# Performance work log

Measured on AMD Instinct MI355X. Metric: run time of the kernel, lower is better.

## Reference

```python
import jax, jax.numpy as jnp
import numpy as np

IMG = 224; PATCH = 16; IN_CH = 3; EMBED = 768
ANCHORS = [(1, 1), (2, 2), (3, 3)]; A = len(ANCHORS)
STRIDE_TOTAL = 16; P = PATCH // STRIDE_TOTAL            # p = 1
PN = IMG // PATCH                                       # 14 patches per side
FH = IMG // STRIDE_TOTAL                                # 14x14 embedding map
G = max(max(a) for a in ANCHORS) * P                    # max roi sampling grid = 3
N = A * PN * PN                                         # 588 anchor scores
J = int((1 - 1 / A) * N)                                # 392 zeroed, matches torch int()
K = N - J                                               # 196 kept boxes
B = 16


def _roi_boxes():
    boxes = []
    for (ah, aw) in ANCHORS:
        h = ah * P; w = aw * P
        for i in range(PN):
            for j in range(PN):
                cy = (P - 1) / 2 + i * P
                cx = (P - 1) / 2 + j * P
                boxes.append([cy - h / 2, cx - w / 2, cy + h / 2, cx + w / 2])
    return np.asarray(boxes, np.float32)

ROI_BOXES = jnp.asarray(_roi_boxes())  # [N, 4], torchvision order (x1,y1,x2,y2)


def conv(x, w, b, s, p):
    y = jax.lax.conv_general_dilated(x, w, (s, s), [(p, p), (p, p)],
                                     dimension_numbers=('NCHW', 'OIHW', 'NCHW'))
    return y + b[None, :, None, None]


def bn(x, g, b, eps=1e-5):
    # training-mode batch norm (biased variance), as in the torch forward
    m = x.mean((0, 2, 3), keepdims=True)
    v = ((x - m) ** 2).mean((0, 2, 3), keepdims=True)
    return g[None, :, None, None] * (x - m) * jax.lax.rsqrt(v + eps) + b[None, :, None, None]


def roi_align_1x1(feat, boxes):
    # torchvision.ops.roi_align, output_size=(1,1), spatial_scale=1, sampling_ratio=-1, aligned=False
    # feat: [B, C, H, W], boxes: [B, K, 4] in (x1, y1, x2, y2)
    Bb, C, H, W = feat.shape
    bx1, by1, bx2, by2 = (boxes[..., i] for i in range(4))
    rw = jnp.maximum(bx2 - bx1, 1.0)
    rh = jnp.maximum(by2 - by1, 1.0)
    gh = jnp.ceil(rh).astype(jnp.int32)                 # adaptive sampling grid
    gw = jnp.ceil(rw).astype(jnp.int32)
    cnt = (gh * gw).astype(feat.dtype)                  # [B, K]
    ii = jnp.arange(G, dtype=feat.dtype)
    ys = by1[..., None] + (ii + 0.5) * rh[..., None] / gh[..., None].astype(feat.dtype)  # [B,K,G]
    xs = bx1[..., None] + (ii + 0.5) * rw[..., None] / gw[..., None].astype(feat.dtype)
    y = jnp.broadcast_to(ys[..., :, None], ys.shape[:-1] + (G, G))  # [B,K,G,G]
    x = jnp.broadcast_to(xs[..., None, :], xs.shape[:-1] + (G, G))
    gmask = (jnp.arange(G)[:, None] < gh[..., None, None]) & (jnp.arange(G)[None, :] < gw[..., None, None])
    valid = (y >= -1.0) & (y <= H) & (x >= -1.0) & (x <= W)
    yc = jnp.maximum(y, 0.0); xc = jnp.maximum(x, 0.0)
    yf = jnp.floor(yc).astype(jnp.int32); xf = jnp.floor(xc).astype(jnp.int32)
    ycap = yf >= H - 1; xcap = xf >= W - 1
    y_lo = jnp.where(ycap, H - 1, yf); y_hi = jnp.where(ycap, H - 1, yf + 1)
    x_lo = jnp.where(xcap, W - 1, xf); x_hi = jnp.where(xcap, W - 1, xf + 1)
    ly = jnp.where(ycap, 0.0, yc - yf.astype(feat.dtype))
    lx = jnp.where(xcap, 0.0, xc - xf.astype(feat.dtype))
    w11 = (1 - ly) * (1 - lx); w12 = (1 - ly) * lx
    w21 = ly * (1 - lx);       w22 = ly * lx
    ff = feat.reshape(Bb, C, H * W)
    gat = jax.vmap(lambda f, i: jnp.take(f, i, axis=-1))  # [C,HW],[K,G,G] -> [C,K,G,G]
    def g(yy, xx):
        return gat(ff, yy * W + xx)
    val = (w11[:, None] * g(y_lo, x_lo) + w12[:, None] * g(y_lo, x_hi)
           + w21[:, None] * g(y_hi, x_lo) + w22[:, None] * g(y_hi, x_hi))
    val = val * (valid & gmask)[:, None].astype(feat.dtype)   # [B,C,K,G,G]
    out = val.sum((-1, -2)) / cnt[:, None, :]                 # [B,C,K]
    return out.transpose(0, 2, 1)                             # [B,K,C]


def _forward(x, pw1, pb1, pw2, pb2, pw3, pb3,
             rw1, rb1, g1, b1, rw2, rb2, g2, b2, rw3, rb3, g3, b3, rw4, rb4):
    Bb = x.shape[0]
    # patch-embed conv stack (no activations, matches nn.Sequential of convs)
    e = conv(x, pw1, pb1, 4, 0)
    e = conv(e, pw2, pb2, 2, 0)
    e = conv(e, pw3, pb3, 2, 0)                    # [B, 768, 14, 14]
    # RPN scoring
    r = jax.nn.relu(bn(conv(x, rw1, rb1, 2, 1), g1, b1))
    r = jax.nn.relu(bn(conv(r, rw2, rb2, 2, 1), g2, b2))
    r = jax.nn.relu(bn(conv(r, rw3, rb3, 2, 1), g3, b3))
    score = conv(r, rw4, rb4, 2, 1)                # [B, A, 14, 14]
    s = score.reshape(Bb, -1)                      # [B, N]
    idx = jnp.argsort(s, axis=-1)                  # ascending, like torch.sort
    onehot = jnp.zeros_like(s).at[jnp.arange(Bb)[:, None], idx].set(
        jnp.broadcast_to((jnp.arange(N) >= J).astype(s.dtype), (Bb, N)))
    sm = jax.nn.softmax(s, axis=1)
    ste = jax.lax.stop_gradient(onehot - sm) + sm  # straight-through estimator
    sel = idx[:, J:]                               # [B, K] kept box ids
    boxes = ROI_BOXES[sel]                         # [B, K, 4]
    emb = roi_align_1x1(e, boxes)                  # [B, K, 768]
    gate = jnp.take_along_axis(ste, sel, axis=1)   # [B, K]
    return emb * gate[..., None]


def setup_inputs():
    key = jax.random.key(0)
    ks = jax.random.split(key, 16)
    def rn(i, shape, s=0.05):
        return jax.random.normal(ks[i], shape, jnp.float32) * s
    return {
        'x': jax.random.normal(ks[0], (B, IN_CH, IMG, IMG), jnp.float32),
        'pw1': rn(1, (64, 3, 4, 4)), 'pb1': rn(2, (64,)),
        'pw2': rn(3, (128, 64, 2, 2)), 'pb2': rn(4, (128,)),
        'pw3': rn(5, (EMBED, 128, 2, 2)), 'pb3': rn(6, (EMBED,)),
        'rw1': rn(7, (64, 3, 3, 3)), 'rb1': rn(8, (64,)),
        'g1': jnp.ones((64,), jnp.float32), 'b1': jnp.zeros((64,), jnp.float32),
        'rw2': rn(9, (128, 64, 3, 3)), 'rb2': rn(10, (128,)),
        'g2': jnp.ones((128,), jnp.float32), 'b2': jnp.zeros((128,), jnp.float32),
        'rw3': rn(11, (256, 128, 3, 3)), 'rb3': rn(12, (256,)),
        'g3': jnp.ones((256,), jnp.float32), 'b3': jnp.zeros((256,), jnp.float32),
        'rw4': rn(13, (A, 256, 3, 3)), 'rb4': rn(14, (A,)),
    }


def reference(x, pw1, pb1, pw2, pb2, pw3, pb3,
              rw1, rb1, g1, b1, rw2, rb2, g2, b2, rw3, rb3, g3, b3, rw4, rb4):
    return _forward(x, pw1, pb1, pw2, pb2, pw3, pb3,
                    rw1, rb1, g1, b1, rw2, rb2, g2, b2, rw3, rb3, g3, b3, rw4, rb4)
```

## Files before the change

kernel.cpp:

```cpp
#include <hip/hip_runtime.h>
#include <math.h>

#define BB 16
#define NBOX 588
#define TOPJ 392
#define TOPK 196
#define EMBED 768
#define NBLK 256

typedef unsigned short u16;
typedef unsigned int   u32;
using short8 = __attribute__((ext_vector_type(8))) short;
using f32x4  = __attribute__((ext_vector_type(4))) float;

__device__ inline u16 rnebf(float x) {
    u32 u = __builtin_bit_cast(u32, x);
    u32 r = u + 0x7fff + ((u >> 16) & 1);
    return (u16)(r >> 16);
}
__device__ inline float bfval(u16 h) {
    u32 u = ((u32)h) << 16;
    return __builtin_bit_cast(float, u);
}
__device__ inline u32 hi2(u32 w0, u32 w1) { return (w0 >> 16) | (w1 & 0xffff0000u); }
__device__ inline u32 lo2(u32 w0, u32 w1) { return (w0 & 0xffffu) | (w1 << 16); }

__global__ void w_split_all(
    const float* __restrict__ rw1, const float* __restrict__ rw2,
    const float* __restrict__ rw3, const float* __restrict__ rw4,
    const float* __restrict__ pw1, const float* __restrict__ pw2,
    const float* __restrict__ pw3,
    float* t1, float* t4, float* q1,
    u16* w2h, u16* w2m, u16* w2l,
    u16* w3h, u16* w3m, u16* w3l,
    u16* p2h, u16* p2l, u16* p3h, u16* p3l)
{
    int i = blockIdx.x * 256 + threadIdx.x;
    if (i < 1728) {
        int oc = i % 64; int k = i / 64; int tap = k % 9; int ic = k / 9;
        t1[i] = rw1[(oc * 3 + ic) * 9 + tap];
        return;
    }
    i -= 1728;
    if (i < 73728) {
        int oc = i / 576; int rem = i - oc * 576; int tap = rem >> 6; int ic = rem & 63;
        float v = rw2[(oc * 64 + ic) * 9 + tap];
        u16 h = rnebf(v); float r = v - bfval(h);
        u16 m = rnebf(r); float r2 = r - bfval(m);
        w2h[i] = h; w2m[i] = m; w2l[i] = rnebf(r2);
        return;
    }
    i -= 73728;
    if (i < 294912) {
        int oc = i / 1152; int rem = i - oc * 1152; int tap = rem >> 7; int ic = rem & 127;
        float v = rw3[(oc * 128 + ic) * 9 + tap];
        u16 h = rnebf(v); float r = v - bfval(h);
        u16 m = rnebf(r); float r2 = r - bfval(m);
        w3h[i] = h; w3m[i] = m; w3l[i] = rnebf(r2);
        return;
    }
    i -= 294912;
    if (i < 6912) {
        int ic = i % 256; int t = i / 256; int tap = t % 9; int oc = t / 9;
        t4[i] = rw4[(oc * 256 + ic) * 9 + tap];
        return;
    }
    i -= 6912;
    if (i < 3072) {
        int oc = i % 64; int k = i / 64; int tap = k % 16; int ic = k / 16;
        q1[i] = pw1[(oc * 3 + ic) * 16 + tap];
        return;
    }
    i -= 3072;
    if (i < 32768) {
        int oc = i >> 8; int rem = i & 255; int tap = rem >> 6; int ic = rem & 63;
        float v = pw2[(oc * 64 + ic) * 4 + tap];
        u16 h = rnebf(v);
        p2h[i] = h; p2l[i] = rnebf(v - bfval(h));
        return;
    }
    i -= 32768;
    if (i < 393216) {
        int oc = i >> 9; int rem = i & 511; int tap = rem >> 7; int ic = rem & 127;
        float v = pw3[(oc * 128 + ic) * 4 + tap];
        u16 h = rnebf(v);
        p3h[i] = h; p3l[i] = rnebf(v - bfval(h));
        return;
    }
}

__global__ void split3_bn(float* __restrict__ x, u16* __restrict__ lp,
                          const float* __restrict__ coef, int Cmask, long n4) {
    long i = (long)blockIdx.x * 256 + threadIdx.x;
    if (i >= n4) return;
    float4 v = *reinterpret_cast<const float4*>(x + i * 4);
    int c0 = (int)((i * 4) & Cmask);
    float4 sc = *reinterpret_cast<const float4*>(coef + c0);
    float4 sh = *reinterpret_cast<const float4*>(coef + (Cmask + 1) + c0);
    float y[4] = {fmaxf(fmaf(v.x, sc.x, sh.x), 0.f), fmaxf(fmaf(v.y, sc.y, sh.y), 0.f),
                  fmaxf(fmaf(v.z, sc.z, sh.z), 0.f), fmaxf(fmaf(v.w, sc.w, sh.w), 0.f)};
    u32 w[4]; u16 l[4];
#pragma unroll
    for (int j = 0; j < 4; ++j) {
        u16 h = rnebf(y[j]); float r = y[j] - bfval(h);
        u16 m = rnebf(r);    float r2 = r - bfval(m);
        l[j] = rnebf(r2);
        w[j] = ((u32)h << 16) | (u32)m;
    }
    uint4 wv; wv.x = w[0]; wv.y = w[1]; wv.z = w[2]; wv.w = w[3];
    *reinterpret_cast<uint4*>(x + i * 4) = wv;
    uint2 lv; lv.x = (u32)l[0] | ((u32)l[1] << 16); lv.y = (u32)l[2] | ((u32)l[3] << 16);
    *reinterpret_cast<uint2*>(lp + i * 4) = lv;
}

__global__ void split2_plain(float* __restrict__ x, long n4) {
    long i = (long)blockIdx.x * 256 + threadIdx.x;
    if (i >= n4) return;
    float4 v = *reinterpret_cast<const float4*>(x + i * 4);
    float y[4] = {v.x, v.y, v.z, v.w};
    u32 w[4];
#pragma unroll
    for (int j = 0; j < 4; ++j) {
        u16 h = rnebf(y[j]);
        u16 l = rnebf(y[j] - bfval(h));
        w[j] = ((u32)h << 16) | (u32)l;
    }
    uint4 wv; wv.x = w[0]; wv.y = w[1]; wv.z = w[2]; wv.w = w[3];
    *reinterpret_cast<uint4*>(x + i * 4) = wv;
}

template<int KH, int KW, int S, int P, int OCT>
__global__ __launch_bounds__(256) void conv_direct_nhwc(
    const float* __restrict__ in, const float* __restrict__ wT,
    const float* __restrict__ bias, float* __restrict__ out,
    int Cin, int Hin, int Win, int Cout, int Hout, int Wout)
{
    const int hw = Hout * Wout;
    const long total = (long)BB * hw;
    long sp = (long)blockIdx.x * 256 + threadIdx.x;
    if (sp >= total) return;
    int b  = (int)(sp / hw);
    int r  = (int)(sp - (long)b * hw);
    int oy = r / Wout;
    int ox = r - oy * Wout;
    int oc0 = blockIdx.y * OCT;

    float acc[OCT];
#pragma unroll
    for (int i = 0; i < OCT; ++i) acc[i] = bias[oc0 + i];

    int  ixc[KW]; long yoff[KH]; float xm[KW], ym[KH];
#pragma unroll
    for (int kx = 0; kx < KW; ++kx) {
        int ix = ox * S - P + kx;
        xm[kx] = (ix >= 0 && ix < Win) ? 1.f : 0.f;
        ixc[kx] = min(max(ix, 0), Win - 1);
    }
#pragma unroll
    for (int ky = 0; ky < KH; ++ky) {
        int iy = oy * S - P + ky;
        ym[ky] = (iy >= 0 && iy < Hin) ? 1.f : 0.f;
        yoff[ky] = (long)min(max(iy, 0), Hin - 1) * Win;
    }

    const float* ib = in + (long)b * Cin * Hin * Win;
    for (int ic = 0; ic < Cin; ++ic) {
        const float* ip = ib + (long)ic * Hin * Win;
#pragma unroll
        for (int ky = 0; ky < KH; ++ky) {
            const float* row = ip + yoff[ky];
#pragma unroll
            for (int kx = 0; kx < KW; ++kx) {
                float v = row[ixc[kx]];
                if (P > 0) v *= ym[ky] * xm[kx];
                const float* wr = wT + ((long)((ic * KH + ky) * KW + kx)) * Cout + oc0;
#pragma unroll
                for (int i = 0; i < OCT; ++i) acc[i] = fmaf(v, wr[i], acc[i]);
            }
        }
    }
    float* op = out + sp * Cout + oc0;
#pragma unroll
    for (int i = 0; i < OCT; i += 4) {
        float4 v = {acc[i], acc[i+1], acc[i+2], acc[i+3]};
        *reinterpret_cast<float4*>(op + i) = v;
    }
}

#define MBM 64
#define MBN 64
template<int KH, int KW, int S, int P, int CLOG, int NS, bool STATS>
__global__ __launch_bounds__(256, 6) void mfma_conv7(
    const u32* __restrict__ hm, const u16* __restrict__ lp,
    const u16* __restrict__ w0, const u16* __restrict__ w1, const u16* __restrict__ w2,
    const float* __restrict__ bias, float* __restrict__ out,
    float* __restrict__ psum, float* __restrict__ psq, int NT,
    int Hin, int Win, int Cout, int Hout, int Wout)
{
    const int Cin = 1 << CLOG;
    const int KK = KH * KW;
    const int Ktot = Cin * KK;
    const int hw = Hout * Wout;
    const long Mtot = (long)BB * hw;

    const int nwg = gridDim.x;
    const int orig = blockIdx.x;
    const int xcd = orig & 7, pos = orig >> 3;
    const int qc = nwg >> 3, rc = nwg & 7;
    const int logical = (xcd < rc ? xcd * (qc + 1) : rc * (qc + 1) + (xcd - rc) * qc) + pos;
    const int MT = nwg / NT;
    const int mt = logical / NT;
    const int nt = logical - mt * NT;
    const int n0 = nt * MBN;
    const long m0 = (long)mt * MBM;

    __shared__ u16 Asm[NS][MBM * 32];
    __shared__ u16 Bsm[NS][MBN * 32];

    const int tid = threadIdx.x;

    const int srow = tid >> 2;
    const int slot = tid & 3;
    long sp_g = m0 + srow; if (sp_g >= Mtot) sp_g = Mtot - 1;
    const int gb  = (int)(sp_g / hw);
    const int gr  = (int)(sp_g - (long)gb * hw);
    const int goy = gr / Wout;
    const int gox = gr - goy * Wout;
    const long ibase_e = (long)gb * Hin * Win * Cin;

    uint4 ga0, ga1, gal, b0r, b1r, b2r;

    auto gatherA = [&](int k0) {
        int tap = k0 >> CLOG;
        int ky = tap / KW, kx = tap - ky * KW;
        int icb = (k0 & (Cin - 1)) + slot * 8;
        int iy = goy * S - P + ky;
        int ix = gox * S - P + kx;
        bool ok = true;
        if (P > 0) {
            ok = (iy >= 0 && iy < Hin && ix >= 0 && ix < Win);
            iy = min(max(iy, 0), Hin - 1);
            ix = min(max(ix, 0), Win - 1);
        }
        long e = ibase_e + ((long)iy * Win + ix) * Cin + icb;
        const uint4* ph = reinterpret_cast<const uint4*>(hm + e);
        ga0 = ph[0]; ga1 = ph[1];
        if constexpr (NS == 3)
            gal = *reinterpret_cast<const uint4*>(lp + e);
        if (P > 0 && !ok) {
            uint4 z; z.x = z.y = z.z = z.w = 0u;
            ga0 = z; ga1 = z;
            if constexpr (NS == 3) gal = z;
        }
    };
    auto gatherB = [&](int k0) {
        long eb = (long)(n0 + srow) * Ktot + k0 + slot * 8;
        b0r = *reinterpret_cast<const uint4*>(w0 + eb);
        b1r = *reinterpret_cast<const uint4*>(w1 + eb);
        if constexpr (NS == 3) b2r = *reinterpret_cast<const uint4*>(w2 + eb);
    };
    auto stage = [&]() {
        const int sw = (srow >> 1) & 3;
        const int o = srow * 32 + ((slot ^ sw) << 3);
        uint4 H, M;
        H.x = hi2(ga0.x, ga0.y); H.y = hi2(ga0.z, ga0.w);
        H.z = hi2(ga1.x, ga1.y); H.w = hi2(ga1.z, ga1.w);
        M.x = lo2(ga0.x, ga0.y); M.y = lo2(ga0.z, ga0.w);
        M.z = lo2(ga1.x, ga1.y); M.w = lo2(ga1.z, ga1.w);
        *reinterpret_cast<uint4*>(&Asm[0][o]) = H;
        *reinterpret_cast<uint4*>(&Asm[1][o]) = M;
        if constexpr (NS == 3) *reinterpret_cast<uint4*>(&Asm[2][o]) = gal;
        *reinterpret_cast<uint4*>(&Bsm[0][o]) = b0r;
        *reinterpret_cast<uint4*>(&Bsm[1][o]) = b1r;
        if constexpr (NS == 3) *reinterpret_cast<uint4*>(&Bsm[2][o]) = b2r;
    };

    const int w    = tid >> 6;
    const int lane = tid & 63;
    const int wr = w >> 1, wc = w & 1;
    const int l15 = lane & 15;
    const int sl  = lane >> 4;

    f32x4 acc[2][2];
#pragma unroll
    for (int f = 0; f < 2; ++f)
#pragma unroll
        for (int g = 0; g < 2; ++g) acc[f][g] = (f32x4){0.f, 0.f, 0.f, 0.f};

    auto computeChunk = [&]() {
        short8 bfr[2][NS];
#pragma unroll
        for (int g = 0; g < 2; ++g) {
            int br = wc * 32 + g * 16 + l15;
            int bo = br * 32 + ((sl ^ ((br >> 1) & 3)) << 3);
#pragma unroll
            for (int s = 0; s < NS; ++s)
                bfr[g][s] = __builtin_bit_cast(short8,
                    *reinterpret_cast<const uint4*>(&Bsm[s][bo]));
        }
#pragma unroll
        for (int f = 0; f < 2; ++f) {
            int ar = wr * 32 + f * 16 + l15;
            int ao = ar * 32 + ((sl ^ ((ar >> 1) & 3)) << 3);
            short8 a0 = __builtin_bit_cast(short8,
                *reinterpret_cast<const uint4*>(&Asm[0][ao]));
            short8 a1 = __builtin_bit_cast(short8,
                *reinterpret_cast<const uint4*>(&Asm[1][ao]));
            short8 a2;
            if constexpr (NS == 3)
                a2 = __builtin_bit_cast(short8,
                    *reinterpret_cast<const uint4*>(&Asm[2][ao]));
#pragma unroll
            for (int g = 0; g < 2; ++g) {
                acc[f][g] = __builtin_amdgcn_mfma_f32_16x16x32_bf16(a0, bfr[g][0], acc[f][g], 0, 0, 0);
                acc[f][g] = __builtin_amdgcn_mfma_f32_16x16x32_bf16(a0, bfr[g][1], acc[f][g], 0, 0, 0);
                acc[f][g] = __builtin_amdgcn_mfma_f32_16x16x32_bf16(a1, bfr[g][0], acc[f][g], 0, 0, 0);
                if constexpr (NS == 3) {
                    acc[f][g] = __builtin_amdgcn_mfma_f32_16x16x32_bf16(a1, bfr[g][1], acc[f][g], 0, 0, 0);
                    acc[f][g] = __builtin_amdgcn_mfma_f32_16x16x32_bf16(a0, bfr[g][2], acc[f][g], 0, 0, 0);
                    acc[f][g] = __builtin_amdgcn_mfma_f32_16x16x32_bf16(a2, bfr[g][0], acc[f][g], 0, 0, 0);
                }
            }
        }
    };

    const int nch = Ktot / 32;
    gatherA(0); gatherB(0);
    for (int c = 0; c < nch; ++c) {
        __syncthreads();
        stage();
        __syncthreads();
        if (c + 1 < nch) { gatherA((c + 1) * 32); gatherB((c + 1) * 32); }
        computeChunk();
    }

    float bv[2];
#pragma unroll
    for (int g = 0; g < 2; ++g) bv[g] = bias[n0 + wc * 32 + g * 16 + l15];
    float ss[2] = {0.f, 0.f}, qq[2] = {0.f, 0.f};
#pragma unroll
    for (int f = 0; f < 2; ++f) {
        long row0 = m0 + wr * 32 + f * 16 + sl * 4;
#pragma unroll
        for (int g = 0; g < 2; ++g) {
            int col = n0 + wc * 32 + g * 16 + l15;
#pragma unroll
            for (int r = 0; r < 4; ++r) {
                long row = row0 + r;
                float y = acc[f][g][r] + bv[g];
                if (row < Mtot) out[row * (long)Cout + col] = y;
                if (STATS) { ss[g] += y; qq[g] += y * y; }
            }
        }
    }
    if (STATS) {
        __syncthreads();
        float* st = reinterpret_cast<float*>(&Asm[0][0]);
        float* sq = st + MBN * 8;
        int slotc = wr * 4 + sl;
#pragma unroll
        for (int g = 0; g < 2; ++g) {
            int cl = wc * 32 + g * 16 + l15;
            st[cl * 8 + slotc] = ss[g];
            sq[cl * 8 + slotc] = qq[g];
        }
        __syncthreads();
        if (tid < MBN) {
            float sAcc = 0.f, qAcc = 0.f;
            for (int j = 0; j < 8; ++j) { sAcc += st[tid * 8 + j]; qAcc += sq[tid * 8 + j]; }
            int c = n0 + tid;
            psum[(long)c * MT + mt] = sAcc;
            psq [(long)c * MT + mt] = qAcc;
        }
    }
}

__global__ void bn_stats_nhwc(const float* __restrict__ x, float* __restrict__ psum,
                              float* __restrict__ psq, int C, int CLOG, long R) {
    const int C4 = C >> 2;
    const int tid = threadIdx.x;
    const int c4 = tid & (C4 - 1);
    const int rg = tid >> (CLOG - 2);
    const int rpb = 256 >> (CLOG - 2);
    float4 s = {0.f, 0.f, 0.f, 0.f}, q = {0.f, 0.f, 0.f, 0.f};
    for (long r = (long)blockIdx.x * rpb + rg; r < R; r += (long)gridDim.x * rpb) {
        float4 v = *reinterpret_cast<const float4*>(x + r * C + c4 * 4);
        s.x += v.x; s.y += v.y; s.z += v.z; s.w += v.w;
        q.x += v.x * v.x; q.y += v.y * v.y; q.z += v.z * v.z; q.w += v.w * v.w;
    }
    __shared__ float4 sd[256], qd[256];
    sd[tid] = s; qd[tid] = q;
    __syncthreads();
    if (tid < C4) {
        float4 Sv = sd[tid], Qv = qd[tid];
        for (int g = 1; g < rpb; ++g) {
            float4 a = sd[tid + g * C4], b = qd[tid + g * C4];
            Sv.x += a.x; Sv.y += a.y; Sv.z += a.z; Sv.w += a.w;
            Qv.x += b.x; Qv.y += b.y; Qv.z += b.z; Qv.w += b.w;
        }
        float Sa[4] = {Sv.x, Sv.y, Sv.z, Sv.w}, Qa[4] = {Qv.x, Qv.y, Qv.z, Qv.w};
        for (int l = 0; l < 4; ++l) {
            psum[(long)(tid * 4 + l) * NBLK + blockIdx.x] = Sa[l];
            psq [(long)(tid * 4 + l) * NBLK + blockIdx.x] = Qa[l];
        }
    }
}

__global__ void bn_coef_par(const float* __restrict__ psum, const float* __restrict__ psq,
                            const float* __restrict__ gamma, const float* __restrict__ beta,
                            float* __restrict__ coef, int C, float inv_cnt, int nparts) {
    int c = blockIdx.x;
    int tid = threadIdx.x;
    float s = 0.f, q = 0.f;
    for (int p = tid; p < nparts; p += 256) {
        s += psum[(long)c * nparts + p];
        q += psq [(long)c * nparts + p];
    }
    __shared__ float sd[256], qd[256];
    sd[tid] = s; qd[tid] = q;
    __syncthreads();
    for (int o = 128; o > 0; o >>= 1) {
        if (tid < o) { sd[tid] += sd[tid + o]; qd[tid] += qd[tid + o]; }
        __syncthreads();
    }
    if (tid == 0) {
        float mean = sd[0] * inv_cnt;
        float var  = qd[0] * inv_cnt - mean * mean;
        float sc = gamma[c] * rsqrtf(var + 1e-5f);
        coef[c] = sc;
        coef[C + c] = beta[c] - mean * sc;
    }
}

__global__ void score_partial(const float* __restrict__ r3, const float* __restrict__ wT4,
                              const float* __restrict__ coef, float* __restrict__ part) {
    int idx = blockIdx.x * 256 + threadIdx.x;
    if (idx >= 9 * 3136) return;
    int tap = idx / 3136;
    int sp  = idx - tap * 3136;
    int b = sp / 196; int pos = sp - b * 196;
    int oy = pos / 14, ox = pos - oy * 14;
    int ky = tap / 3, kx = tap - ky * 3;
    int iy = oy * 2 - 1 + ky, ix = ox * 2 - 1 + kx;
    float mval = (iy >= 0 && iy < 28 && ix >= 0 && ix < 28) ? 1.f : 0.f;
    iy = min(max(iy, 0), 27); ix = min(max(ix, 0), 27);
    const float* p = r3 + ((long)(b * 28 + iy) * 28 + ix) * 256;
    float a0 = 0.f, a1 = 0.f, a2 = 0.f;
    for (int icv = 0; icv < 64; ++icv) {
        float4 v  = *reinterpret_cast<const float4*>(p + icv * 4);
        float4 sc = *reinterpret_cast<const float4*>(coef + icv * 4);
        float4 sh = *reinterpret_cast<const float4*>(coef + 256 + icv * 4);
        float u[4];
        u[0] = fmaxf(fmaf(v.x, sc.x, sh.x), 0.f);
        u[1] = fmaxf(fmaf(v.y, sc.y, sh.y), 0.f);
        u[2] = fmaxf(fmaf(v.z, sc.z, sh.z), 0.f);
        u[3] = fmaxf(fmaf(v.w, sc.w, sh.w), 0.f);
        float4 w0 = *reinterpret_cast<const float4*>(wT4 + ((0 * 9 + tap) * 256 + icv * 4));
        float4 w1 = *reinterpret_cast<const float4*>(wT4 + ((1 * 9 + tap) * 256 + icv * 4));
        float4 w2 = *reinterpret_cast<const float4*>(wT4 + ((2 * 9 + tap) * 256 + icv * 4));
        a0 += u[0]*w0.x + u[1]*w0.y + u[2]*w0.z + u[3]*w0.w;
        a1 += u[0]*w1.x + u[1]*w1.y + u[2]*w1.z + u[3]*w1.w;
        a2 += u[0]*w2.x + u[1]*w2.y + u[2]*w2.z + u[3]*w2.w;
    }
    part[idx * 3 + 0] = a0 * mval;
    part[idx * 3 + 1] = a1 * mval;
    part[idx * 3 + 2] = a2 * mval;
}

__global__ void score_reduce(const float* __restrict__ part, const float* __restrict__ rb4,
                             float* __restrict__ score) {
    int idx = blockIdx.x * 256 + threadIdx.x;
    if (idx >= 9408) return;
    int sp = idx / 3; int oc = idx - sp * 3;
    float s = rb4[oc];
    for (int t = 0; t < 9; ++t) s += part[((long)t * 3136 + sp) * 3 + oc];
    int b = sp / 196, pos = sp - b * 196;
    score[b * NBOX + oc * 196 + pos] = s;
}

__global__ void topk_kernel(const float* __restrict__ score, int* __restrict__ sel,
                            float* __restrict__ gate) {
    int b = blockIdx.x;
    int tid = threadIdx.x;
    __shared__ float s[NBOX];
    __shared__ float red[4];
    for (int n = tid; n < NBOX; n += blockDim.x) s[n] = score[b * NBOX + n];
    __syncthreads();

    float mx = -3.0e38f;
    for (int n = tid; n < NBOX; n += blockDim.x) mx = fmaxf(mx, s[n]);
    for (int o = 32; o > 0; o >>= 1) mx = fmaxf(mx, __shfl_down(mx, o));
    if ((tid & 63) == 0) red[tid >> 6] = mx;
    __syncthreads();
    mx = fmaxf(fmaxf(red[0], red[1]), fmaxf(red[2], red[3]));
    __syncthreads();

    float se = 0.f;
    for (int n = tid; n < NBOX; n += blockDim.x) se += expf(s[n] - mx);
    for (int o = 32; o > 0; o >>= 1) se += __shfl_down(se, o);
    if ((tid & 63) == 0) red[tid >> 6] = se;
    __syncthreads();
    se = red[0] + red[1] + red[2] + red[3];

    for (int n = tid; n < NBOX; n += blockDim.x) {
        float v = s[n];
        int rank = 0;
        for (int m = 0; m < NBOX; ++m) {
            float u = s[m];
            rank += (u < v) || (u == v && m < n);
        }
        if (rank >= TOPJ) {
            int k = rank - TOPJ;
            float p = expf(v - mx) / se;
            sel [b * TOPK + k] = n;
            gate[b * TOPK + k] = (1.0f - p) + p;
        }
    }
}

__global__ void roi_gather(const float* __restrict__ e3, const int* __restrict__ sel,
                           const float* __restrict__ gate, float* __restrict__ out) {
    int bk = blockIdx.x;
    int b = bk / TOPK;
    int n = sel[bk];
    float gt = gate[bk];
    int a   = n / 196;
    int pos = n % 196;
    int i = pos / 14;
    int j = pos % 14;
    int S = a + 1;
    float inv_cnt = 1.0f / (float)(S * S);

    __shared__ int   cidx[9][4];
    __shared__ float cw  [9][4];
    if (threadIdx.x == 0) {
        int t = 0;
        for (int p = 0; p < S; ++p) {
            float yy = (float)j - S * 0.5f + p + 0.5f;
            float yc = fmaxf(yy, 0.0f);
            int yf = (int)floorf(yc);
            int y_lo, y_hi; float ly;
            if (yf >= 13) { y_lo = 13; y_hi = 13; ly = 0.f; }
            else          { y_lo = yf; y_hi = yf + 1; ly = yc - (float)yf; }
            for (int q = 0; q < S; ++q) {
                float xx = (float)i - S * 0.5f + q + 0.5f;
                float xc = fmaxf(xx, 0.0f);
                int xf = (int)floorf(xc);
                int x_lo, x_hi; float lx;
                if (xf >= 13) { x_lo = 13; x_hi = 13; lx = 0.f; }
                else          { x_lo = xf; x_hi = xf + 1; lx = xc - (float)xf; }
                cidx[t][0] = y_lo * 14 + x_lo;  cw[t][0] = (1.f - ly) * (1.f - lx);
                cidx[t][1] = y_lo * 14 + x_hi;  cw[t][1] = (1.f - ly) * lx;
                cidx[t][2] = y_hi * 14 + x_lo;  cw[t][2] = ly * (1.f - lx);
                cidx[t][3] = y_hi * 14 + x_hi;  cw[t][3] = ly * lx;
                ++t;
            }
        }
    }
    __syncthreads();
    int NS2 = S * S;
    const float* base = e3 + (long)b * 196 * EMBED;
    for (int c = threadIdx.x; c < EMBED; c += blockDim.x) {
        float acc = 0.f;
        for (int t = 0; t < NS2; ++t) {
            acc += cw[t][0] * base[cidx[t][0] * EMBED + c]
                 + cw[t][1] * base[cidx[t][1] * EMBED + c]
                 + cw[t][2] * base[cidx[t][2] * EMBED + c]
                 + cw[t][3] * base[cidx[t][3] * EMBED + c];
        }
        out[(long)bk * EMBED + c] = acc * inv_cnt * gt;
    }
}

extern "C" void kernel_launch(void* const* d_in, const int* in_sizes, int n_in,
                              void* d_out, int out_size, void* d_ws, size_t ws_size,
                              hipStream_t stream) {
    const float* x   = (const float*)d_in[0];
    const float* pw1 = (const float*)d_in[1];
    const float* pb1 = (const float*)d_in[2];
    const float* pw2 = (const float*)d_in[3];
    const float* pb2 = (const float*)d_in[4];
    const float* pw3 = (const float*)d_in[5];
    const float* pb3 = (const float*)d_in[6];
    const float* rw1 = (const float*)d_in[7];
    const float* rb1 = (const float*)d_in[8];
    const float* g1  = (const float*)d_in[9];
    const float* b1  = (const float*)d_in[10];
    const float* rw2 = (const float*)d_in[11];
    const float* rb2 = (const float*)d_in[12];
    const float* g2  = (const float*)d_in[13];
    const float* b2  = (const float*)d_in[14];
    const float* rw3 = (const float*)d_in[15];
    const float* rb3 = (const float*)d_in[16];
    const float* g3  = (const float*)d_in[17];
    const float* b3  = (const float*)d_in[18];
    const float* rw4 = (const float*)d_in[19];
    const float* rb4 = (const float*)d_in[20];

    float* ws = (float*)d_ws;
    const long OFF_R1  = 0;
    const long OFF_R1L = 12845056;
    const long OFF_R2  = 19267584;
    const long OFF_S   = 25690112;

    float* r1   = ws + OFF_R1;
    u16*   r1l  = (u16*)(ws + OFF_R1L);
    float* r2   = ws + OFF_R2;
    u16*   r2l  = (u16*)(ws + OFF_R1L);
    float* r3   = ws + OFF_R1;
    float* e1   = ws + OFF_R1 + 3211264;
    float* e2   = ws + OFF_R1 + 6422528;
    float* e3   = ws + OFF_R1 + 8028160;

    float* score = ws + OFF_S;
    float* psum  = score + 9408;
    float* psq   = psum + 100352;
    float* coef  = psq + 100352;
    float* gate  = coef + 512;
    int*   sel   = (int*)(gate + 3136);
    float* partSP = ws + OFF_R1L;

    float* dout = (float*)d_out;
    float* t_rw1 = dout;
    float* t_rw4 = dout + 1728;
    float* q_pw1 = dout + 8640;
    u16* w2h = (u16*)(dout + 11712);
    u16* w2m = (u16*)(dout + 48576);
    u16* w2l = (u16*)(dout + 85440);
    u16* w3h = (u16*)(dout + 122304);
    u16* w3m = (u16*)(dout + 269760);
    u16* w3l = (u16*)(dout + 417216);
    u16* p2h = (u16*)(dout + 564672);
    u16* p2l = (u16*)(dout + 581056);
    u16* p3h = (u16*)(dout + 597440);
    u16* p3l = (u16*)(dout + 794048);

    const int T = 256;
    w_split_all<<<3150, T, 0, stream>>>(rw1, rw2, rw3, rw4, pw1, pw2, pw3,
                                        t_rw1, t_rw4, q_pw1,
                                        w2h, w2m, w2l, w3h, w3m, w3l,
                                        p2h, p2l, p3h, p3l);

    conv_direct_nhwc<3,3,2,1,16><<<dim3(784, 4), T, 0, stream>>>(
        x, t_rw1, rb1, r1, 3, 224, 224, 64, 112, 112);
    bn_stats_nhwc<<<NBLK, T, 0, stream>>>(r1, psum, psq, 64, 6, 200704);
    bn_coef_par<<<64, T, 0, stream>>>(psum, psq, g1, b1, coef, 64, 1.0f / 200704.f, NBLK);
    split3_bn<<<12544, T, 0, stream>>>(r1, r1l, coef, 63, 3211264);

    mfma_conv7<3,3,2,1,6,3,true><<<1568, T, 0, stream>>>(
        (const u32*)r1, r1l, w2h, w2m, w2l, rb2, r2, psum, psq, 2,
        112, 112, 128, 56, 56);
    bn_coef_par<<<128, T, 0, stream>>>(psum, psq, g2, b2, coef, 128, 1.0f / 50176.f, 784);
    split3_bn<<<6272, T, 0, stream>>>(r2, r2l, coef, 127, 1605632);

    mfma_conv7<3,3,2,1,7,3,true><<<784, T, 0, stream>>>(
        (const u32*)r2, r2l, w3h, w3m, w3l, rb3, r3, psum, psq, 4,
        56, 56, 256, 28, 28);
    bn_coef_par<<<256, T, 0, stream>>>(psum, psq, g3, b3, coef, 256, 1.0f / 12544.f, 196);

    score_partial<<<(9 * 3136 + T - 1) / T, T, 0, stream>>>(r3, t_rw4, coef, partSP);
    score_reduce<<<(9408 + T - 1) / T, T, 0, stream>>>(partSP, rb4, score);

    topk_kernel<<<16, T, 0, stream>>>(score, sel, gate);

    conv_direct_nhwc<4,4,4,0,16><<<dim3(196, 4), T, 0, stream>>>(
        x, q_pw1, pb1, e1, 3, 224, 224, 64, 56, 56);
    split2_plain<<<3136, T, 0, stream>>>(e1, 802816);
    mfma_conv7<2,2,2,0,6,2,false><<<392, T, 0, stream>>>(
        (const u32*)e1, nullptr, p2h, p2l, nullptr, pb2, e2, nullptr, nullptr, 2,
        56, 56, 128, 28, 28);
    split2_plain<<<1568, T, 0, stream>>>(e2, 401408);
    mfma_conv7<2,2,2,0,7,2,false><<<588, T, 0, stream>>>(
        (const u32*)e2, nullptr, p3h, p3l, nullptr, pb3, e3, nullptr, nullptr, 12,
        28, 28, 768, 14, 14);

    roi_gather<<<16 * TOPK, T, 0, stream>>>(e3, sel, gate, (float*)d_out);
}
```

Before: 339.3 us.

## Read conv weights directly from global, narrow N tiles, retune direct conv tiling

New measurement: 456.9 us. +34.6%, slower.

```diff
diff --git a/kernel.cpp b/kernel.cpp
--- a/kernel.cpp
+++ b/kernel.cpp
@@ -187,10 +187,8 @@
     }
 }
 
-#define MBM 64
-#define MBN 64
-template<int KH, int KW, int S, int P, int CLOG, int NS, bool STATS>
-__global__ __launch_bounds__(256, 6) void mfma_conv7(
+template<int KH, int KW, int S, int P, int CLOG, int NS, bool STATS, int BN, int MINW>
+__global__ __launch_bounds__(256, MINW) void mfma_conv8(
     const u32* __restrict__ hm, const u16* __restrict__ lp,
     const u16* __restrict__ w0, const u16* __restrict__ w1, const u16* __restrict__ w2,
     const float* __restrict__ bias, float* __restrict__ out,
@@ -202,6 +200,8 @@
     const int Ktot = Cin * KK;
     const int hw = Hout * Wout;
     const long Mtot = (long)BB * hw;
+    constexpr int WCW = BN / 2;
+    constexpr int GC  = WCW / 16;
 
     const int nwg = gridDim.x;
     const int orig = blockIdx.x;
@@ -211,11 +211,10 @@
     const int MT = nwg / NT;
     const int mt = logical / NT;
     const int nt = logical - mt * NT;
-    const int n0 = nt * MBN;
-    const long m0 = (long)mt * MBM;
-
-    __shared__ u16 Asm[NS][MBM * 32];
-    __shared__ u16 Bsm[NS][MBN * 32];
+    const int n0 = nt * BN;
+    const long m0 = (long)mt * 64;
+
+    __shared__ u16 Asm[NS][64 * 32];
 
     const int tid = threadIdx.x;
 
@@ -228,7 +227,7 @@
     const int gox = gr - goy * Wout;
     const long ibase_e = (long)gb * Hin * Win * Cin;
 
-    uint4 ga0, ga1, gal, b0r, b1r, b2r;
+    uint4 ga0, ga1, gal;
 
     auto gatherA = [&](int k0) {
         int tap = k0 >> CLOG;
@@ -252,12 +251,6 @@
             ga0 = z; ga1 = z;
             if constexpr (NS == 3) gal = z;
         }
-    };
-    auto gatherB = [&](int k0) {
-        long eb = (long)(n0 + srow) * Ktot + k0 + slot * 8;
-        b0r = *reinterpret_cast<const uint4*>(w0 + eb);
-        b1r = *reinterpret_cast<const uint4*>(w1 + eb);
-        if constexpr (NS == 3) b2r = *reinterpret_cast<const uint4*>(w2 + eb);
     };
     auto stage = [&]() {
         const int sw = (srow >> 1) & 3;
@@ -270,9 +263,6 @@
         *reinterpret_cast<uint4*>(&Asm[0][o]) = H;
         *reinterpret_cast<uint4*>(&Asm[1][o]) = M;
         if constexpr (NS == 3) *reinterpret_cast<uint4*>(&Asm[2][o]) = gal;
-        *reinterpret_cast<uint4*>(&Bsm[0][o]) = b0r;
-        *reinterpret_cast<uint4*>(&Bsm[1][o]) = b1r;
-        if constexpr (NS == 3) *reinterpret_cast<uint4*>(&Bsm[2][o]) = b2r;
     };
 
     const int w    = tid >> 6;
@@ -281,22 +271,24 @@
     const int l15 = lane & 15;
     const int sl  = lane >> 4;
 
-    f32x4 acc[2][2];
+    f32x4 acc[2][GC];
 #pragma unroll
     for (int f = 0; f < 2; ++f)
 #pragma unroll
-        for (int g = 0; g < 2; ++g) acc[f][g] = (f32x4){0.f, 0.f, 0.f, 0.f};
-
-    auto computeChunk = [&]() {
-        short8 bfr[2][NS];
-#pragma unroll
-        for (int g = 0; g < 2; ++g) {
-            int br = wc * 32 + g * 16 + l15;
-            int bo = br * 32 + ((sl ^ ((br >> 1) & 3)) << 3);
-#pragma unroll
-            for (int s = 0; s < NS; ++s)
-                bfr[g][s] = __builtin_bit_cast(short8,
-                    *reinterpret_cast<const uint4*>(&Bsm[s][bo]));
+        for (int g = 0; g < GC; ++g) acc[f][g] = (f32x4){0.f, 0.f, 0.f, 0.f};
+
+    auto computeChunk = [&](int kc) {
+        short8 bfr[GC][NS];
+#pragma unroll
+        for (int g = 0; g < GC; ++g) {
+            long rowb = (long)(n0 + wc * WCW + g * 16 + l15) * Ktot + kc + sl * 8;
+            bfr[g][0] = __builtin_bit_cast(short8,
+                *reinterpret_cast<const uint4*>(w0 + rowb));
+            bfr[g][1] = __builtin_bit_cast(short8,
+                *reinterpret_cast<const uint4*>(w1 + rowb));
+            if constexpr (NS == 3)
+                bfr[g][2] = __builtin_bit_cast(short8,
+                    *reinterpret_cast<const uint4*>(w2 + rowb));
         }
 #pragma unroll
         for (int f = 0; f < 2; ++f) {
@@ -311,7 +303,7 @@
                 a2 = __builtin_bit_cast(short8,
                     *reinterpret_cast<const uint4*>(&Asm[2][ao]));
 #pragma unroll
-            for (int g = 0; g < 2; ++g) {
+            for (int g = 0; g < GC; ++g) {
                 acc[f][g] = __builtin_amdgcn_mfma_f32_16x16x32_bf16(a0, bfr[g][0], acc[f][g], 0, 0, 0);
                 acc[f][g] = __builtin_amdgcn_mfma_f32_16x16x32_bf16(a0, bfr[g][1], acc[f][g], 0, 0, 0);
                 acc[f][g] = __builtin_amdgcn_mfma_f32_16x16x32_bf16(a1, bfr[g][0], acc[f][g], 0, 0, 0);
@@ -325,25 +317,27 @@
     };
 
     const int nch = Ktot / 32;
-    gatherA(0); gatherB(0);
+    gatherA(0);
     for (int c = 0; c < nch; ++c) {
         __syncthreads();
         stage();
         __syncthreads();
-        if (c + 1 < nch) { gatherA((c + 1) * 32); gatherB((c + 1) * 32); }
-        computeChunk();
-    }
-
-    float bv[2];
-#pragma unroll
-    for (int g = 0; g < 2; ++g) bv[g] = bias[n0 + wc * 32 + g * 16 + l15];
-    float ss[2] = {0.f, 0.f}, qq[2] = {0.f, 0.f};
+        if (c + 1 < nch) gatherA((c + 1) * 32);
+        computeChunk(c * 32);
+    }
+
+    float bv[GC];
+#pragma unroll
+    for (int g = 0; g < GC; ++g) bv[g] = bias[n0 + wc * WCW + g * 16 + l15];
+    float ss[GC], qq[GC];
+#pragma unroll
+    for (int g = 0; g < GC; ++g) { ss[g] = 0.f; qq[g] = 0.f; }
 #pragma unroll
     for (int f = 0; f < 2; ++f) {
         long row0 = m0 + wr * 32 + f * 16 + sl * 4;
 #pragma unroll
-        for (int g = 0; g < 2; ++g) {
-            int col = n0 + wc * 32 + g * 16 + l15;
+        for (int g = 0; g < GC; ++g) {
+            int col = n0 + wc * WCW + g * 16 + l15;
 #pragma unroll
             for (int r = 0; r < 4; ++r) {
                 long row = row0 + r;
@@ -356,16 +350,16 @@
     if (STATS) {
         __syncthreads();
         float* st = reinterpret_cast<float*>(&Asm[0][0]);
-        float* sq = st + MBN * 8;
+        float* sq = st + BN * 8;
         int slotc = wr * 4 + sl;
 #pragma unroll
-        for (int g = 0; g < 2; ++g) {
-            int cl = wc * 32 + g * 16 + l15;
+        for (int g = 0; g < GC; ++g) {
+            int cl = wc * WCW + g * 16 + l15;
             st[cl * 8 + slotc] = ss[g];
             sq[cl * 8 + slotc] = qq[g];
         }
         __syncthreads();
-        if (tid < MBN) {
+        if (tid < BN) {
             float sAcc = 0.f, qAcc = 0.f;
             for (int j = 0; j < 8; ++j) { sAcc += st[tid * 8 + j]; qAcc += sq[tid * 8 + j]; }
             int c = n0 + tid;
@@ -641,20 +635,20 @@
                                         w2h, w2m, w2l, w3h, w3m, w3l,
                                         p2h, p2l, p3h, p3l);
 
-    conv_direct_nhwc<3,3,2,1,16><<<dim3(784, 4), T, 0, stream>>>(
+    conv_direct_nhwc<3,3,2,1,32><<<dim3(784, 2), T, 0, stream>>>(
         x, t_rw1, rb1, r1, 3, 224, 224, 64, 112, 112);
     bn_stats_nhwc<<<NBLK, T, 0, stream>>>(r1, psum, psq, 64, 6, 200704);
     bn_coef_par<<<64, T, 0, stream>>>(psum, psq, g1, b1, coef, 64, 1.0f / 200704.f, NBLK);
     split3_bn<<<12544, T, 0, stream>>>(r1, r1l, coef, 63, 3211264);
 
-    mfma_conv7<3,3,2,1,6,3,true><<<1568, T, 0, stream>>>(
+    mfma_conv8<3,3,2,1,6,3,true,64,6><<<1568, T, 0, stream>>>(
         (const u32*)r1, r1l, w2h, w2m, w2l, rb2, r2, psum, psq, 2,
         112, 112, 128, 56, 56);
     bn_coef_par<<<128, T, 0, stream>>>(psum, psq, g2, b2, coef, 128, 1.0f / 50176.f, 784);
     split3_bn<<<6272, T, 0, stream>>>(r2, r2l, coef, 127, 1605632);
 
-    mfma_conv7<3,3,2,1,7,3,true><<<784, T, 0, stream>>>(
-        (const u32*)r2, r2l, w3h, w3m, w3l, rb3, r3, psum, psq, 4,
+    mfma_conv8<3,3,2,1,7,3,true,32,6><<<1568, T, 0, stream>>>(
+        (const u32*)r2, r2l, w3h, w3m, w3l, rb3, r3, psum, psq, 8,
         56, 56, 256, 28, 28);
     bn_coef_par<<<256, T, 0, stream>>>(psum, psq, g3, b3, coef, 256, 1.0f / 12544.f, 196);
 
@@ -663,15 +657,15 @@
 
     topk_kernel<<<16, T, 0, stream>>>(score, sel, gate);
 
-    conv_direct_nhwc<4,4,4,0,16><<<dim3(196, 4), T, 0, stream>>>(
+    conv_direct_nhwc<4,4,4,0,32><<<dim3(196, 2), T, 0, stream>>>(
         x, q_pw1, pb1, e1, 3, 224, 224, 64, 56, 56);
     split2_plain<<<3136, T, 0, stream>>>(e1, 802816);
-    mfma_conv7<2,2,2,0,6,2,false><<<392, T, 0, stream>>>(
-        (const u32*)e1, nullptr, p2h, p2l, nullptr, pb2, e2, nullptr, nullptr, 2,
+    mfma_conv8<2,2,2,0,6,2,false,32,8><<<784, T, 0, stream>>>(
+        (const u32*)e1, nullptr, p2h, p2l, nullptr, pb2, e2, nullptr, nullptr, 4,
         56, 56, 128, 28, 28);
     split2_plain<<<1568, T, 0, stream>>>(e2, 401408);
-    mfma_conv7<2,2,2,0,7,2,false><<<588, T, 0, stream>>>(
-        (const u32*)e2, nullptr, p3h, p3l, nullptr, pb3, e3, nullptr, nullptr, 12,
+    mfma_conv8<2,2,2,0,7,2,false,32,8><<<1176, T, 0, stream>>>(
+        (const u32*)e2, nullptr, p3h, p3l, nullptr, pb3, e3, nullptr, nullptr, 24,
         28, 28, 768, 14, 14);
 
     roi_gather<<<16 * TOPK, T, 0, stream>>>(e3, sel, gate, (float*)d_out);
```
